# Optimization experiments

Measured on AMD Instinct MI355X. Metric: run time of the kernel, lower is better.

Reference implementation:

```python
import jax, jax.numpy as jnp
import numpy as np

N_NODES = 50000
N_EDGES = 600000
D = 128          # in_dim == hiddim
C = 40           # n_classes
L = 4            # n GCN layers
EPS = 1e-5       # BatchNorm1d default eps


def setup_inputs() -> dict:
    key = jax.random.key(0)
    ks = jax.random.split(key, 5)
    h = jax.random.normal(ks[0], (N_NODES, D), jnp.float32)
    src = jax.random.randint(ks[1], (N_EDGES,), 0, N_NODES, jnp.int32)
    dst = jax.random.randint(ks[2], (N_EDGES,), 0, N_NODES, jnp.int32)
    # learned parameters
    bn_gamma = jnp.ones((D,), jnp.float32)
    bn_beta = jnp.zeros((D,), jnp.float32)
    W1 = jax.random.normal(ks[3], (D, D), jnp.float32) * (1.0 / np.sqrt(D))
    b1 = jnp.zeros((D,), jnp.float32)
    bn2_gamma = jnp.ones((D,), jnp.float32)
    bn2_beta = jnp.zeros((D,), jnp.float32)
    W2 = jax.random.normal(ks[4], (D, C), jnp.float32) * (1.0 / np.sqrt(D))
    b2 = jnp.zeros((C,), jnp.float32)
    return {"h": h, "src": src, "dst": dst,
            "bn_gamma": bn_gamma, "bn_beta": bn_beta,
            "W1": W1, "b1": b1,
            "bn2_gamma": bn2_gamma, "bn2_beta": bn2_beta,
            "W2": W2, "b2": b2}


def _batchnorm(x, gamma, beta):
    # BatchNorm1d in training mode: biased batch variance over the node axis
    mu = x.mean(axis=0)
    var = x.var(axis=0)
    return (x - mu) * jax.lax.rsqrt(var + EPS) * gamma + beta


def reference(h, src, dst, bn_gamma, bn_beta, W1, b1, bn2_gamma, bn2_beta, W2, b2):
    n = h.shape[0]
    # in-degrees from dst indices, clamped to >= 1 (matches g.in_degrees().clamp(min=1))
    deg = jax.ops.segment_sum(jnp.ones(dst.shape[0], jnp.float32), dst, num_segments=n)
    norm = jax.lax.rsqrt(jnp.maximum(deg, 1.0))[:, None]  # deg^{-0.5}, [N,1]
    # in_feat_dropout = 0.0 -> identity
    for _ in range(L):
        h = h * norm
        # copy_u + sum reducer: scatter-add source features into destination nodes
        h = jax.ops.segment_sum(h[src], dst, num_segments=n)
        h = h * norm
        h = jax.nn.relu(_batchnorm(h, bn_gamma, bn_beta))  # shared BN across layers
    # MultiLinearLayer: Linear -> BN -> Linear (activation=None)
    x = h @ W1 + b1
    x = _batchnorm(x, bn2_gamma, bn2_beta)
    return x @ W2 + b2
```

## Files before the change

### kernel.cpp

```cpp
#include <hip/hip_runtime.h>

#define N_NODESC 50000
#define N_EDGESC 600000
#define DDIM 128
#define NCLASS 40
#define BN_EPS 1e-5f
#define STAT_BLOCKS 196
#define GATHER_BLOCKS 2048
#define SORT_ROWS 128
#define SORT_CAP 2560
#define SORT_BLOCKS 391

typedef short bhalf8 __attribute__((ext_vector_type(8)));
typedef float f32x4 __attribute__((ext_vector_type(4)));

union ABfrag { bhalf8 v; unsigned short u[8]; uint4 q; };

__device__ inline float bflo(unsigned d) { return __builtin_bit_cast(float, d << 16); }
__device__ inline float bfhi(unsigned d) { return __builtin_bit_cast(float, d & 0xffff0000u); }
__device__ inline unsigned short f2bf(float f) {
    unsigned u = __builtin_bit_cast(unsigned, f);
    u += 0x7fffu + ((u >> 16) & 1u);
    return (unsigned short)(u >> 16);
}

__global__ __launch_bounds__(256) void deg_kernel(const int* __restrict__ dst, int* __restrict__ deg) {
    int e = blockIdx.x * 256 + threadIdx.x;
    if (e < N_EDGESC) atomicAdd(&deg[dst[e]], 1);
}

__global__ __launch_bounds__(256) void scan1_kernel(const int* __restrict__ deg,
                                                    int* __restrict__ rowptr,
                                                    int* __restrict__ blocksums) {
    __shared__ int sh[256];
    int t = threadIdx.x;
    int i = blockIdx.x * 256 + t;
    int v = (i < N_NODESC) ? deg[i] : 0;
    sh[t] = v;
    __syncthreads();
    #pragma unroll
    for (int off = 1; off < 256; off <<= 1) {
        int tv = (t >= off) ? sh[t - off] : 0;
        __syncthreads();
        sh[t] += tv;
        __syncthreads();
    }
    if (i < N_NODESC) rowptr[i] = sh[t] - v;
    if (t == 255) blocksums[blockIdx.x] = sh[255];
}

__global__ void scan2_kernel(const int* __restrict__ blocksums, int* __restrict__ blockoff) {
    __shared__ int sh[256];
    int t = threadIdx.x;
    int v = (t < STAT_BLOCKS) ? blocksums[t] : 0;
    sh[t] = v;
    __syncthreads();
    #pragma unroll
    for (int off = 1; off < 256; off <<= 1) {
        int tv = (t >= off) ? sh[t - off] : 0;
        __syncthreads();
        sh[t] += tv;
        __syncthreads();
    }
    blockoff[t] = sh[t] - v;
}

__global__ __launch_bounds__(256) void scan3_kernel(int* __restrict__ rowptr,
                                                    const int* __restrict__ blockoff,
                                                    const int* __restrict__ deg,
                                                    int* __restrict__ cursor,
                                                    float* __restrict__ nrm) {
    int i = blockIdx.x * 256 + threadIdx.x;
    if (i < N_NODESC) {
        int r = rowptr[i] + blockoff[blockIdx.x];
        rowptr[i] = r;
        cursor[i] = r;
        nrm[i] = rsqrtf(fmaxf((float)deg[i], 1.0f));
    }
    if (blockIdx.x == 0 && threadIdx.x == 0) rowptr[N_NODESC] = N_EDGESC;
}

__global__ __launch_bounds__(256) void fill_kernel(const int* __restrict__ src,
                                                   const int* __restrict__ dst,
                                                   int* __restrict__ cursor,
                                                   int* __restrict__ csr) {
    int e = blockIdx.x * 256 + threadIdx.x;
    if (e < N_EDGESC) {
        int d = dst[e];
        int p = atomicAdd(&cursor[d], 1);
        csr[p] = src[e];
    }
}

__global__ __launch_bounds__(128) void sortrows_kernel(const int* __restrict__ rowptr,
                                                       int* __restrict__ csr) {
    __shared__ int buf[SORT_CAP];
    int r0 = blockIdx.x * SORT_ROWS;
    int r1 = r0 + SORT_ROWS; if (r1 > N_NODESC) r1 = N_NODESC;
    int base = rowptr[r0];
    int end  = rowptr[r1];
    int cnt  = end - base;
    if (cnt <= SORT_CAP) {
        for (int j = threadIdx.x; j < cnt; j += 128) buf[j] = csr[base + j];
        __syncthreads();
        int i = r0 + threadIdx.x;
        if (i < r1) {
            int b = rowptr[i] - base, e = rowptr[i + 1] - base;
            for (int j = b + 1; j < e; j++) {
                int v = buf[j];
                int k = j - 1;
                while (k >= b && buf[k] > v) { buf[k + 1] = buf[k]; k--; }
                buf[k + 1] = v;
            }
        }
        __syncthreads();
        for (int j = threadIdx.x; j < cnt; j += 128) csr[base + j] = buf[j];
    } else {
        int i = r0 + threadIdx.x;
        if (i < r1) {
            int b = rowptr[i], e = rowptr[i + 1];
            for (int j = b + 1; j < e; j++) {
                int v = csr[j];
                int k = j - 1;
                while (k >= b && csr[k] > v) { csr[k + 1] = csr[k]; k--; }
                csr[k + 1] = v;
            }
        }
    }
}

__global__ __launch_bounds__(256) void hconv_kernel(const float* __restrict__ h,
                                                    unsigned short* __restrict__ out) {
    int i = blockIdx.x * 256 + threadIdx.x;
    if (i < N_NODESC * DDIM / 8) {
        float4 v0 = reinterpret_cast<const float4*>(h)[i * 2];
        float4 v1 = reinterpret_cast<const float4*>(h)[i * 2 + 1];
        uint4 p;
        p.x = (unsigned)f2bf(v0.x) | ((unsigned)f2bf(v0.y) << 16);
        p.y = (unsigned)f2bf(v0.z) | ((unsigned)f2bf(v0.w) << 16);
        p.z = (unsigned)f2bf(v1.x) | ((unsigned)f2bf(v1.y) << 16);
        p.w = (unsigned)f2bf(v1.z) | ((unsigned)f2bf(v1.w) << 16);
        reinterpret_cast<uint4*>(out)[i] = p;
    }
}

__global__ __launch_bounds__(256) void w1prep_kernel(const float* __restrict__ W1,
                                                     unsigned short* __restrict__ W1T) {
    int idx = blockIdx.x * 256 + threadIdx.x;
    if (idx < DDIM * DDIM) {
        int k = idx >> 7, n = idx & 127;
        W1T[n * DDIM + k] = f2bf(W1[idx]);
    }
}

template <bool BN>
__global__ __launch_bounds__(256) void gather_kernel(const unsigned short* __restrict__ in,
                                                     const float* __restrict__ nrm,
                                                     const int* __restrict__ rowptr,
                                                     const int* __restrict__ csr,
                                                     const float* __restrict__ mu,
                                                     const float* __restrict__ rstd,
                                                     const float* __restrict__ gamma,
                                                     const float* __restrict__ beta,
                                                     unsigned short* __restrict__ out) {
    int lane = threadIdx.x & 63;
    int wave = threadIdx.x >> 6;
    int q    = lane >> 4;
    int c    = lane & 15;
    float sc[8], sh[8];
    if (BN) {
        float4 m0 = *reinterpret_cast<const float4*>(mu + c * 8);
        float4 m1 = *reinterpret_cast<const float4*>(mu + c * 8 + 4);
        float4 r0 = *reinterpret_cast<const float4*>(rstd + c * 8);
        float4 r1 = *reinterpret_cast<const float4*>(rstd + c * 8 + 4);
        float4 g0 = *reinterpret_cast<const float4*>(gamma + c * 8);
        float4 g1 = *reinterpret_cast<const float4*>(gamma + c * 8 + 4);
        float4 b0 = *reinterpret_cast<const float4*>(beta + c * 8);
        float4 b1 = *reinterpret_cast<const float4*>(beta + c * 8 + 4);
        sc[0] = r0.x * g0.x; sc[1] = r0.y * g0.y; sc[2] = r0.z * g0.z; sc[3] = r0.w * g0.w;
        sc[4] = r1.x * g1.x; sc[5] = r1.y * g1.y; sc[6] = r1.z * g1.z; sc[7] = r1.w * g1.w;
        sh[0] = b0.x - m0.x * sc[0]; sh[1] = b0.y - m0.y * sc[1];
        sh[2] = b0.z - m0.z * sc[2]; sh[3] = b0.w - m0.w * sc[3];
        sh[4] = b1.x - m1.x * sc[4]; sh[5] = b1.y - m1.y * sc[5];
        sh[6] = b1.z - m1.z * sc[6]; sh[7] = b1.w - m1.w * sc[7];
    }
    for (int i = blockIdx.x * 4 + wave; i < N_NODESC; i += GATHER_BLOCKS * 4) {
        int b = rowptr[i], e = rowptr[i + 1];
        float a[8] = {0.f, 0.f, 0.f, 0.f, 0.f, 0.f, 0.f, 0.f};
        int j = b + q;
        if (j < e) {
            int sidx = csr[j];
            float ns  = nrm[sidx];
            uint4 d   = reinterpret_cast<const uint4*>(in + (size_t)sidx * DDIM)[c];
            for (j += 4;; j += 4) {
                bool more = (j < e);
                int nsidx = 0; float nns = 0.f;
                uint4 nd = make_uint4(0u, 0u, 0u, 0u);
                if (more) {
                    nsidx = csr[j];
                    nns   = nrm[nsidx];
                    nd    = reinterpret_cast<const uint4*>(in + (size_t)nsidx * DDIM)[c];
                }
                float f[8];
                f[0] = bflo(d.x); f[1] = bfhi(d.x);
                f[2] = bflo(d.y); f[3] = bfhi(d.y);
                f[4] = bflo(d.z); f[5] = bfhi(d.z);
                f[6] = bflo(d.w); f[7] = bfhi(d.w);
                #pragma unroll
                for (int t = 0; t < 8; t++) {
                    float v = BN ? fmaxf(f[t] * sc[t] + sh[t], 0.f) : f[t];
                    a[t] += v * ns;
                }
                if (!more) break;
                d = nd; ns = nns;
            }
        }
        #pragma unroll
        for (int t = 0; t < 8; t++) a[t] += __shfl_xor(a[t], 16);
        #pragma unroll
        for (int t = 0; t < 8; t++) a[t] += __shfl_xor(a[t], 32);
        if (q == 0) {
            float ni = nrm[i];
            uint4 p;
            p.x = (unsigned)f2bf(a[0] * ni) | ((unsigned)f2bf(a[1] * ni) << 16);
            p.y = (unsigned)f2bf(a[2] * ni) | ((unsigned)f2bf(a[3] * ni) << 16);
            p.z = (unsigned)f2bf(a[4] * ni) | ((unsigned)f2bf(a[5] * ni) << 16);
            p.w = (unsigned)f2bf(a[6] * ni) | ((unsigned)f2bf(a[7] * ni) << 16);
            reinterpret_cast<uint4*>(out + (size_t)i * DDIM)[c] = p;
        }
    }
}

__global__ __launch_bounds__(256) void stats_bf16_kernel(const unsigned short* __restrict__ x,
                                                         float* __restrict__ partials) {
    __shared__ float sh[256];
    int c2 = threadIdx.x & 63;
    int rg = threadIdx.x >> 6;
    int row0 = blockIdx.x * 256;
    int rowEnd = row0 + 256; if (rowEnd > N_NODESC) rowEnd = N_NODESC;
    float s0 = 0.f, s1 = 0.f, q0 = 0.f, q1 = 0.f;
    for (int r = row0 + rg; r < rowEnd; r += 4) {
        unsigned d = reinterpret_cast<const unsigned*>(x + (size_t)r * DDIM)[c2];
        float f0 = bflo(d), f1 = bfhi(d);
        s0 += f0; q0 += f0 * f0;
        s1 += f1; q1 += f1 * f1;
    }
    sh[threadIdx.x] = s0; __syncthreads();
    if (rg == 0) s0 += sh[64 + c2] + sh[128 + c2] + sh[192 + c2];
    __syncthreads();
    sh[threadIdx.x] = s1; __syncthreads();
    if (rg == 0) s1 += sh[64 + c2] + sh[128 + c2] + sh[192 + c2];
    __syncthreads();
    sh[threadIdx.x] = q0; __syncthreads();
    if (rg == 0) q0 += sh[64 + c2] + sh[128 + c2] + sh[192 + c2];
    __syncthreads();
    sh[threadIdx.x] = q1; __syncthreads();
    if (rg == 0) {
        q1 += sh[64 + c2] + sh[128 + c2] + sh[192 + c2];
        partials[blockIdx.x * 256 + 2 * c2]           = s0;
        partials[blockIdx.x * 256 + 2 * c2 + 1]       = s1;
        partials[blockIdx.x * 256 + 128 + 2 * c2]     = q0;
        partials[blockIdx.x * 256 + 128 + 2 * c2 + 1] = q1;
    }
}

__global__ __launch_bounds__(256) void stats_f32_kernel(const float* __restrict__ x,
                                                        float* __restrict__ partials) {
    __shared__ float sh[256];
    int col = threadIdx.x & 127;
    int grp = threadIdx.x >> 7;
    int rowEnd = (blockIdx.x + 1) * 256;
    if (rowEnd > N_NODESC) rowEnd = N_NODESC;
    float s = 0.f, q = 0.f;
    for (int r = blockIdx.x * 256 + grp; r < rowEnd; r += 2) {
        float v = x[(size_t)r * DDIM + col];
        s += v;
        q += v * v;
    }
    sh[threadIdx.x] = s;
    __syncthreads();
    float s2 = (grp == 0) ? (s + sh[128 + col]) : 0.f;
    __syncthreads();
    sh[threadIdx.x] = q;
    __syncthreads();
    if (grp == 0) {
        float q2 = q + sh[128 + col];
        partials[blockIdx.x * 256 + col]       = s2;
        partials[blockIdx.x * 256 + 128 + col] = q2;
    }
}

__global__ __launch_bounds__(1024) void finalize_kernel(const float* __restrict__ partials,
                                                        float* __restrict__ mu, float* __restrict__ rstd) {
    __shared__ double shd[2048];
    int col = threadIdx.x & 127;
    int sl  = threadIdx.x >> 7;
    double s = 0.0, q = 0.0;
    for (int b = sl; b < STAT_BLOCKS; b += 8) {
        s += (double)partials[b * 256 + col];
        q += (double)partials[b * 256 + 128 + col];
    }
    shd[threadIdx.x] = s;
    shd[1024 + threadIdx.x] = q;
    __syncthreads();
    if (sl == 0) {
        #pragma unroll
        for (int k = 1; k < 8; k++) {
            s += shd[k * 128 + col];
            q += shd[1024 + k * 128 + col];
        }
        double m = s / (double)N_NODESC;
        double v = q / (double)N_NODESC - m * m;
        if (v < 0.0) v = 0.0;
        mu[col]   = (float)m;
        rstd[col] = rsqrtf((float)v + BN_EPS);
    }
}

__global__ __launch_bounds__(256) void linear1_mfma(const unsigned short* __restrict__ Qb,
                                                    const unsigned short* __restrict__ W1T,
                                                    const float* __restrict__ b1,
                                                    const float* __restrict__ mu,
                                                    const float* __restrict__ rstd,
                                                    const float* __restrict__ gamma,
                                                    const float* __restrict__ beta,
                                                    float* __restrict__ X) {
    __shared__ uint4 wlds[2048];
    __shared__ float scs[DDIM], shs[DDIM], bias[DDIM];
    int tid = threadIdx.x;
    for (int i = tid; i < 2048; i += 256) {
        uint4 v = reinterpret_cast<const uint4*>(W1T)[i];
        int o = i << 4;
        int n = o >> 8;
        int sw = (o & 255) ^ ((n & 7) << 4);
        wlds[(n << 4) | (sw >> 4)] = v;
    }
    if (tid < DDIM) {
        float a = rstd[tid] * gamma[tid];
        scs[tid] = a;
        shs[tid] = beta[tid] - mu[tid] * a;
        bias[tid] = b1[tid];
    }
    __syncthreads();
    int wave = tid >> 6, lane = tid & 63;
    int l15 = lane & 15, l4 = lane >> 4;
    int tile = blockIdx.x * 4 + wave;
    if (tile >= 3128) return;
    int row0 = tile * 16;
    int arow = row0 + l15; if (arow >= N_NODESC) arow = N_NODESC - 1;
    const uint4* aptr = reinterpret_cast<const uint4*>(Qb + (size_t)arow * DDIM);
    f32x4 acc[8];
    #pragma unroll
    for (int cf = 0; cf < 8; cf++) acc[cf] = (f32x4){0.f, 0.f, 0.f, 0.f};
    #pragma unroll
    for (int ks = 0; ks < 4; ks++) {
        uint4 ad = aptr[ks * 4 + l4];
        int kb = ks * 32 + l4 * 8;
        ABfrag a;
        float f;
        f = bflo(ad.x); a.u[0] = f2bf(fmaxf(f * scs[kb + 0] + shs[kb + 0], 0.f));
        f = bfhi(ad.x); a.u[1] = f2bf(fmaxf(f * scs[kb + 1] + shs[kb + 1], 0.f));
        f = bflo(ad.y); a.u[2] = f2bf(fmaxf(f * scs[kb + 2] + shs[kb + 2], 0.f));
        f = bfhi(ad.y); a.u[3] = f2bf(fmaxf(f * scs[kb + 3] + shs[kb + 3], 0.f));
        f = bflo(ad.z); a.u[4] = f2bf(fmaxf(f * scs[kb + 4] + shs[kb + 4], 0.f));
        f = bfhi(ad.z); a.u[5] = f2bf(fmaxf(f * scs[kb + 5] + shs[kb + 5], 0.f));
        f = bflo(ad.w); a.u[6] = f2bf(fmaxf(f * scs[kb + 6] + shs[kb + 6], 0.f));
        f = bfhi(ad.w); a.u[7] = f2bf(fmaxf(f * scs[kb + 7] + shs[kb + 7], 0.f));
        int koff = ks * 64 + l4 * 16;
        #pragma unroll
        for (int cf = 0; cf < 8; cf++) {
            int n = cf * 16 + l15;
            ABfrag b;
            b.q = wlds[(n << 4) | ((koff ^ ((n & 7) << 4)) >> 4)];
            acc[cf] = __builtin_amdgcn_mfma_f32_16x16x32_bf16(a.v, b.v, acc[cf], 0, 0, 0);
        }
    }
    #pragma unroll
    for (int cf = 0; cf < 8; cf++) {
        int col = cf * 16 + l15;
        float bb = bias[col];
        #pragma unroll
        for (int r = 0; r < 4; r++) {
            int row = row0 + l4 * 4 + r;
            if (row < N_NODESC) X[(size_t)row * DDIM + col] = acc[cf][r] + bb;
        }
    }
}

__global__ void fold_kernel(const float* __restrict__ W2, const float* __restrict__ b2,
                            const float* __restrict__ g2, const float* __restrict__ be2,
                            const float* __restrict__ mu2, const float* __restrict__ rstd2,
                            float* __restrict__ W2f, float* __restrict__ b2f) {
    __shared__ float s[DDIM], t[DDIM];
    int tid = threadIdx.x;
    if (tid < DDIM) {
        float sc = rstd2[tid] * g2[tid];
        s[tid] = sc;
        t[tid] = be2[tid] - mu2[tid] * sc;
    }
    __syncthreads();
    for (int idx = tid; idx < DDIM * NCLASS; idx += 256) {
        int k = idx / NCLASS;
        W2f[idx] = W2[idx] * s[k];
    }
    if (tid < NCLASS) {
        float acc = b2[tid];
        for (int k = 0; k < DDIM; k++) acc += t[k] * W2[k * NCLASS + tid];
        b2f[tid] = acc;
    }
}

#define L2_TILE 64
__global__ __launch_bounds__(256) void linear2_kernel(const float* __restrict__ X,
                                                      const float* __restrict__ W2f,
                                                      const float* __restrict__ b2f,
                                                      float* __restrict__ out) {
    __shared__ float Ws[DDIM][NCLASS];
    for (int idx = threadIdx.x; idx < DDIM * NCLASS; idx += 256) {
        (&Ws[0][0])[idx] = W2f[idx];
    }
    __syncthreads();
    int cg = threadIdx.x & 7;
    int rp = threadIdx.x >> 3;
    int c0 = cg * 5;
    for (int base = blockIdx.x * L2_TILE; base < N_NODESC; base += gridDim.x * L2_TILE) {
        int row0 = base + rp * 2;
        int row1 = row0 + 1;
        int r0c = row0 < N_NODESC ? row0 : (N_NODESC - 1);
        int r1c = row1 < N_NODESC ? row1 : (N_NODESC - 1);
        const float* r0p = X + (size_t)r0c * DDIM;
        const float* r1p = X + (size_t)r1c * DDIM;
        float a0[5] = {0.f, 0.f, 0.f, 0.f, 0.f};
        float a1[5] = {0.f, 0.f, 0.f, 0.f, 0.f};
        #pragma unroll 4
        for (int k4 = 0; k4 < DDIM; k4 += 4) {
            float4 x0 = *reinterpret_cast<const float4*>(r0p + k4);
            float4 x1 = *reinterpret_cast<const float4*>(r1p + k4);
            #pragma unroll
            for (int j = 0; j < 5; j++) {
                float w0 = Ws[k4 + 0][c0 + j];
                float w1 = Ws[k4 + 1][c0 + j];
                float w2 = Ws[k4 + 2][c0 + j];
                float w3 = Ws[k4 + 3][c0 + j];
                a0[j] += w0 * x0.x + w1 * x0.y + w2 * x0.z + w3 * x0.w;
                a1[j] += w0 * x1.x + w1 * x1.y + w2 * x1.z + w3 * x1.w;
            }
        }
        if (row0 < N_NODESC) {
            #pragma unroll
            for (int j = 0; j < 5; j++) out[(size_t)row0 * NCLASS + c0 + j] = a0[j] + b2f[c0 + j];
        }
        if (row1 < N_NODESC) {
            #pragma unroll
            for (int j = 0; j < 5; j++) out[(size_t)row1 * NCLASS + c0 + j] = a1[j] + b2f[c0 + j];
        }
    }
}

extern "C" void kernel_launch(void* const* d_in, const int* in_sizes, int n_in,
                              void* d_out, int out_size, void* d_ws, size_t ws_size,
                              hipStream_t stream) {
    const float* h    = (const float*)d_in[0];
    const int*   src  = (const int*)d_in[1];
    const int*   dst  = (const int*)d_in[2];
    const float* bn_g = (const float*)d_in[3];
    const float* bn_b = (const float*)d_in[4];
    const float* W1   = (const float*)d_in[5];
    const float* b1   = (const float*)d_in[6];
    const float* g2   = (const float*)d_in[7];
    const float* be2  = (const float*)d_in[8];
    const float* W2   = (const float*)d_in[9];
    const float* b2   = (const float*)d_in[10];
    float* out = (float*)d_out;

    float* ws      = (float*)d_ws;
    float* nrm     = ws;
    int*   deg     = (int*)(ws + N_NODESC);
    int*   cursor  = deg + N_NODESC;
    int*   rowptr  = cursor + N_NODESC;
    int*   bsums   = rowptr + 50016;
    int*   boff    = bsums + 256;
    int*   csr     = boff + 256;
    float* partials = (float*)(csr + N_EDGESC);
    float* mu      = partials + STAT_BLOCKS * 256;
    float* rstd    = mu + DDIM;
    float* W2f     = rstd + DDIM;
    float* b2f     = W2f + DDIM * NCLASS;
    unsigned short* W1T = (unsigned short*)(b2f + 64);
    unsigned short* Hb  = (unsigned short*)((float*)W1T + 8192);
    unsigned short* Pb  = (unsigned short*)((float*)Hb + 3200000);
    float* X       = (float*)((float*)Pb + 3200000);

    (void)in_sizes; (void)n_in; (void)out_size; (void)ws_size;

    hipMemsetAsync(deg, 0, N_NODESC * sizeof(int), stream);
    deg_kernel<<<(N_EDGESC + 255) / 256, 256, 0, stream>>>(dst, deg);
    scan1_kernel<<<STAT_BLOCKS, 256, 0, stream>>>(deg, rowptr, bsums);
    scan2_kernel<<<1, 256, 0, stream>>>(bsums, boff);
    scan3_kernel<<<STAT_BLOCKS, 256, 0, stream>>>(rowptr, boff, deg, cursor, nrm);
    fill_kernel<<<(N_EDGESC + 255) / 256, 256, 0, stream>>>(src, dst, cursor, csr);
    sortrows_kernel<<<SORT_BLOCKS, 128, 0, stream>>>(rowptr, csr);
    hconv_kernel<<<(N_NODESC * DDIM / 8 + 255) / 256, 256, 0, stream>>>(h, Hb);
    w1prep_kernel<<<(DDIM * DDIM + 255) / 256, 256, 0, stream>>>(W1, W1T);

    gather_kernel<false><<<GATHER_BLOCKS, 256, 0, stream>>>(Hb, nrm, rowptr, csr,
                                                            nullptr, nullptr, nullptr, nullptr, Pb);
    stats_bf16_kernel<<<STAT_BLOCKS, 256, 0, stream>>>(Pb, partials);
    finalize_kernel<<<1, 1024, 0, stream>>>(partials, mu, rstd);
    gather_kernel<true><<<GATHER_BLOCKS, 256, 0, stream>>>(Pb, nrm, rowptr, csr,
                                                           mu, rstd, bn_g, bn_b, Hb);
    stats_bf16_kernel<<<STAT_BLOCKS, 256, 0, stream>>>(Hb, partials);
    finalize_kernel<<<1, 1024, 0, stream>>>(partials, mu, rstd);
    gather_kernel<true><<<GATHER_BLOCKS, 256, 0, stream>>>(Hb, nrm, rowptr, csr,
                                                           mu, rstd, bn_g, bn_b, Pb);
    stats_bf16_kernel<<<STAT_BLOCKS, 256, 0, stream>>>(Pb, partials);
    finalize_kernel<<<1, 1024, 0, stream>>>(partials, mu, rstd);
    gather_kernel<true><<<GATHER_BLOCKS, 256, 0, stream>>>(Pb, nrm, rowptr, csr,
                                                           mu, rstd, bn_g, bn_b, Hb);
    stats_bf16_kernel<<<STAT_BLOCKS, 256, 0, stream>>>(Hb, partials);
    finalize_kernel<<<1, 1024, 0, stream>>>(partials, mu, rstd);

    linear1_mfma<<<782, 256, 0, stream>>>(Hb, W1T, b1, mu, rstd, bn_g, bn_b, X);
    stats_f32_kernel<<<STAT_BLOCKS, 256, 0, stream>>>(X, partials);
    finalize_kernel<<<1, 1024, 0, stream>>>(partials, mu, rstd);
    fold_kernel<<<1, 256, 0, stream>>>(W2, b2, g2, be2, mu, rstd, W2f, b2f);
    linear2_kernel<<<512, 256, 0, stream>>>(X, W2f, b2f, out);
}
```

Baseline: 429.4 us.

## Fuse BatchNorm statistics into gather and linear1 kernels, column-chunk the gather

The separate stats passes over each layer output are removed. BatchNorm sum and sum-of-squares are now accumulated inside the gather kernel and the linear1 MFMA kernel, which write per-block partials for new finalize kernels. The gather is also restructured so each block handles one 32-column chunk of the feature dimension, with 16 edge slots per wave, which changes how memory is accessed. This saves a full re-read of the activations per layer but adds shuffles and LDS reductions, and statistics are now computed from fp32 values rather than the stored bf16.

After: 626.6 us. 1.46x slower.

```diff
diff --git a/kernel.cpp b/kernel.cpp
--- a/kernel.cpp
+++ b/kernel.cpp
@@ -6,7 +6,9 @@
 #define NCLASS 40
 #define BN_EPS 1e-5f
 #define STAT_BLOCKS 196
+#define CHUNK_BLOCKS 512
 #define GATHER_BLOCKS 2048
+#define L1_BLOCKS 782
 #define SORT_ROWS 128
 #define SORT_CAP 2560
 #define SORT_BLOCKS 391
@@ -162,21 +164,27 @@
                                                      const float* __restrict__ rstd,
                                                      const float* __restrict__ gamma,
                                                      const float* __restrict__ beta,
-                                                     unsigned short* __restrict__ out) {
-    int lane = threadIdx.x & 63;
-    int wave = threadIdx.x >> 6;
-    int q    = lane >> 4;
-    int c    = lane & 15;
+                                                     unsigned short* __restrict__ out,
+                                                     float* __restrict__ partials) {
+    __shared__ float red[4][64];
+    int bx    = blockIdx.x;
+    int chunk = bx >> 9;
+    int blk   = bx & (CHUNK_BLOCKS - 1);
+    int lane  = threadIdx.x & 63;
+    int wave  = threadIdx.x >> 6;
+    int slot  = lane >> 2;
+    int cl    = lane & 3;
+    int colbase = chunk * 32 + cl * 8;
     float sc[8], sh[8];
     if (BN) {
-        float4 m0 = *reinterpret_cast<const float4*>(mu + c * 8);
-        float4 m1 = *reinterpret_cast<const float4*>(mu + c * 8 + 4);
-        float4 r0 = *reinterpret_cast<const float4*>(rstd + c * 8);
-        float4 r1 = *reinterpret_cast<const float4*>(rstd + c * 8 + 4);
-        float4 g0 = *reinterpret_cast<const float4*>(gamma + c * 8);
-        float4 g1 = *reinterpret_cast<const float4*>(gamma + c * 8 + 4);
-        float4 b0 = *reinterpret_cast<const float4*>(beta + c * 8);
-        float4 b1 = *reinterpret_cast<const float4*>(beta + c * 8 + 4);
+        float4 m0 = *reinterpret_cast<const float4*>(mu + colbase);
+        float4 m1 = *reinterpret_cast<const float4*>(mu + colbase + 4);
+        float4 r0 = *reinterpret_cast<const float4*>(rstd + colbase);
+        float4 r1 = *reinterpret_cast<const float4*>(rstd + colbase + 4);
+        float4 g0 = *reinterpret_cast<const float4*>(gamma + colbase);
+        float4 g1 = *reinterpret_cast<const float4*>(gamma + colbase + 4);
+        float4 b0 = *reinterpret_cast<const float4*>(beta + colbase);
+        float4 b1 = *reinterpret_cast<const float4*>(beta + colbase + 4);
         sc[0] = r0.x * g0.x; sc[1] = r0.y * g0.y; sc[2] = r0.z * g0.z; sc[3] = r0.w * g0.w;
         sc[4] = r1.x * g1.x; sc[5] = r1.y * g1.y; sc[6] = r1.z * g1.z; sc[7] = r1.w * g1.w;
         sh[0] = b0.x - m0.x * sc[0]; sh[1] = b0.y - m0.y * sc[1];
@@ -184,121 +192,101 @@
         sh[4] = b1.x - m1.x * sc[4]; sh[5] = b1.y - m1.y * sc[5];
         sh[6] = b1.z - m1.z * sc[6]; sh[7] = b1.w - m1.w * sc[7];
     }
-    for (int i = blockIdx.x * 4 + wave; i < N_NODESC; i += GATHER_BLOCKS * 4) {
+    float ssum[8] = {0.f,0.f,0.f,0.f,0.f,0.f,0.f,0.f};
+    float sqr[8]  = {0.f,0.f,0.f,0.f,0.f,0.f,0.f,0.f};
+    for (int i = blk * 4 + wave; i < N_NODESC; i += GATHER_BLOCKS / 4 * 4) {
         int b = rowptr[i], e = rowptr[i + 1];
-        float a[8] = {0.f, 0.f, 0.f, 0.f, 0.f, 0.f, 0.f, 0.f};
-        int j = b + q;
-        if (j < e) {
+        float a[8] = {0.f,0.f,0.f,0.f,0.f,0.f,0.f,0.f};
+        for (int j = b + slot; j < e; j += 16) {
             int sidx = csr[j];
-            float ns  = nrm[sidx];
-            uint4 d   = reinterpret_cast<const uint4*>(in + (size_t)sidx * DDIM)[c];
-            for (j += 4;; j += 4) {
-                bool more = (j < e);
-                int nsidx = 0; float nns = 0.f;
-                uint4 nd = make_uint4(0u, 0u, 0u, 0u);
-                if (more) {
-                    nsidx = csr[j];
-                    nns   = nrm[nsidx];
-                    nd    = reinterpret_cast<const uint4*>(in + (size_t)nsidx * DDIM)[c];
-                }
-                float f[8];
-                f[0] = bflo(d.x); f[1] = bfhi(d.x);
-                f[2] = bflo(d.y); f[3] = bfhi(d.y);
-                f[4] = bflo(d.z); f[5] = bfhi(d.z);
-                f[6] = bflo(d.w); f[7] = bfhi(d.w);
-                #pragma unroll
-                for (int t = 0; t < 8; t++) {
-                    float v = BN ? fmaxf(f[t] * sc[t] + sh[t], 0.f) : f[t];
-                    a[t] += v * ns;
-                }
-                if (!more) break;
-                d = nd; ns = nns;
+            float ns = nrm[sidx];
+            uint4 d = *reinterpret_cast<const uint4*>(in + (size_t)sidx * DDIM + colbase);
+            float f[8];
+            f[0] = bflo(d.x); f[1] = bfhi(d.x);
+            f[2] = bflo(d.y); f[3] = bfhi(d.y);
+            f[4] = bflo(d.z); f[5] = bfhi(d.z);
+            f[6] = bflo(d.w); f[7] = bfhi(d.w);
+            #pragma unroll
+            for (int t = 0; t < 8; t++) {
+                float v = BN ? fmaxf(f[t] * sc[t] + sh[t], 0.f) : f[t];
+                a[t] += v * ns;
             }
         }
         #pragma unroll
-        for (int t = 0; t < 8; t++) a[t] += __shfl_xor(a[t], 16);
-        #pragma unroll
-        for (int t = 0; t < 8; t++) a[t] += __shfl_xor(a[t], 32);
-        if (q == 0) {
+        for (int t = 0; t < 8; t++) {
+            a[t] += __shfl_xor(a[t], 4);
+            a[t] += __shfl_xor(a[t], 8);
+            a[t] += __shfl_xor(a[t], 16);
+            a[t] += __shfl_xor(a[t], 32);
+        }
+        if (slot == 0) {
             float ni = nrm[i];
+            #pragma unroll
+            for (int t = 0; t < 8; t++) {
+                a[t] *= ni;
+                ssum[t] += a[t];
+                sqr[t]  += a[t] * a[t];
+            }
             uint4 p;
-            p.x = (unsigned)f2bf(a[0] * ni) | ((unsigned)f2bf(a[1] * ni) << 16);
-            p.y = (unsigned)f2bf(a[2] * ni) | ((unsigned)f2bf(a[3] * ni) << 16);
-            p.z = (unsigned)f2bf(a[4] * ni) | ((unsigned)f2bf(a[5] * ni) << 16);
-            p.w = (unsigned)f2bf(a[6] * ni) | ((unsigned)f2bf(a[7] * ni) << 16);
-            reinterpret_cast<uint4*>(out + (size_t)i * DDIM)[c] = p;
-        }
-    }
-}
-
-__global__ __launch_bounds__(256) void stats_bf16_kernel(const unsigned short* __restrict__ x,
-                                                         float* __restrict__ partials) {
-    __shared__ float sh[256];
-    int c2 = threadIdx.x & 63;
-    int rg = threadIdx.x >> 6;
-    int row0 = blockIdx.x * 256;
-    int rowEnd = row0 + 256; if (rowEnd > N_NODESC) rowEnd = N_NODESC;
-    float s0 = 0.f, s1 = 0.f, q0 = 0.f, q1 = 0.f;
-    for (int r = row0 + rg; r < rowEnd; r += 4) {
-        unsigned d = reinterpret_cast<const unsigned*>(x + (size_t)r * DDIM)[c2];
-        float f0 = bflo(d), f1 = bfhi(d);
-        s0 += f0; q0 += f0 * f0;
-        s1 += f1; q1 += f1 * f1;
-    }
-    sh[threadIdx.x] = s0; __syncthreads();
-    if (rg == 0) s0 += sh[64 + c2] + sh[128 + c2] + sh[192 + c2];
-    __syncthreads();
-    sh[threadIdx.x] = s1; __syncthreads();
-    if (rg == 0) s1 += sh[64 + c2] + sh[128 + c2] + sh[192 + c2];
-    __syncthreads();
-    sh[threadIdx.x] = q0; __syncthreads();
-    if (rg == 0) q0 += sh[64 + c2] + sh[128 + c2] + sh[192 + c2];
-    __syncthreads();
-    sh[threadIdx.x] = q1; __syncthreads();
-    if (rg == 0) {
-        q1 += sh[64 + c2] + sh[128 + c2] + sh[192 + c2];
-        partials[blockIdx.x * 256 + 2 * c2]           = s0;
-        partials[blockIdx.x * 256 + 2 * c2 + 1]       = s1;
-        partials[blockIdx.x * 256 + 128 + 2 * c2]     = q0;
-        partials[blockIdx.x * 256 + 128 + 2 * c2 + 1] = q1;
-    }
-}
-
-__global__ __launch_bounds__(256) void stats_f32_kernel(const float* __restrict__ x,
-                                                        float* __restrict__ partials) {
-    __shared__ float sh[256];
+            p.x = (unsigned)f2bf(a[0]) | ((unsigned)f2bf(a[1]) << 16);
+            p.y = (unsigned)f2bf(a[2]) | ((unsigned)f2bf(a[3]) << 16);
+            p.z = (unsigned)f2bf(a[4]) | ((unsigned)f2bf(a[5]) << 16);
+            p.w = (unsigned)f2bf(a[6]) | ((unsigned)f2bf(a[7]) << 16);
+            *reinterpret_cast<uint4*>(out + (size_t)i * DDIM + colbase) = p;
+        }
+    }
+    if (slot == 0) {
+        #pragma unroll
+        for (int t = 0; t < 8; t++) {
+            red[wave][cl * 8 + t]      = ssum[t];
+            red[wave][32 + cl * 8 + t] = sqr[t];
+        }
+    }
+    __syncthreads();
+    int tid = threadIdx.x;
+    if (tid < 64) {
+        partials[(size_t)bx * 64 + tid] = red[0][tid] + red[1][tid] + red[2][tid] + red[3][tid];
+    }
+}
+
+__global__ __launch_bounds__(1024) void finalize_g_kernel(const float* __restrict__ partials,
+                                                          float* __restrict__ mu, float* __restrict__ rstd) {
+    __shared__ double shd[2048];
     int col = threadIdx.x & 127;
-    int grp = threadIdx.x >> 7;
-    int rowEnd = (blockIdx.x + 1) * 256;
-    if (rowEnd > N_NODESC) rowEnd = N_NODESC;
-    float s = 0.f, q = 0.f;
-    for (int r = blockIdx.x * 256 + grp; r < rowEnd; r += 2) {
-        float v = x[(size_t)r * DDIM + col];
-        s += v;
-        q += v * v;
-    }
-    sh[threadIdx.x] = s;
-    __syncthreads();
-    float s2 = (grp == 0) ? (s + sh[128 + col]) : 0.f;
-    __syncthreads();
-    sh[threadIdx.x] = q;
-    __syncthreads();
-    if (grp == 0) {
-        float q2 = q + sh[128 + col];
-        partials[blockIdx.x * 256 + col]       = s2;
-        partials[blockIdx.x * 256 + 128 + col] = q2;
-    }
-}
-
-__global__ __launch_bounds__(1024) void finalize_kernel(const float* __restrict__ partials,
-                                                        float* __restrict__ mu, float* __restrict__ rstd) {
+    int sl  = threadIdx.x >> 7;
+    int ch  = col >> 5, c32 = col & 31;
+    double s = 0.0, q = 0.0;
+    for (int b = sl; b < CHUNK_BLOCKS; b += 8) {
+        const float* p = partials + (size_t)(ch * CHUNK_BLOCKS + b) * 64;
+        s += (double)p[c32];
+        q += (double)p[32 + c32];
+    }
+    shd[threadIdx.x] = s;
+    shd[1024 + threadIdx.x] = q;
+    __syncthreads();
+    if (sl == 0) {
+        #pragma unroll
+        for (int k = 1; k < 8; k++) {
+            s += shd[k * 128 + col];
+            q += shd[1024 + k * 128 + col];
+        }
+        double m = s / (double)N_NODESC;
+        double v = q / (double)N_NODESC - m * m;
+        if (v < 0.0) v = 0.0;
+        mu[col]   = (float)m;
+        rstd[col] = rsqrtf((float)v + BN_EPS);
+    }
+}
+
+__global__ __launch_bounds__(1024) void finalize_l1_kernel(const float* __restrict__ partials,
+                                                           float* __restrict__ mu, float* __restrict__ rstd) {
     __shared__ double shd[2048];
     int col = threadIdx.x & 127;
     int sl  = threadIdx.x >> 7;
     double s = 0.0, q = 0.0;
-    for (int b = sl; b < STAT_BLOCKS; b += 8) {
-        s += (double)partials[b * 256 + col];
-        q += (double)partials[b * 256 + 128 + col];
+    for (int b = sl; b < L1_BLOCKS; b += 8) {
+        s += (double)partials[(size_t)b * 256 + col];
+        q += (double)partials[(size_t)b * 256 + 128 + col];
     }
     shd[threadIdx.x] = s;
     shd[1024 + threadIdx.x] = q;
@@ -324,9 +312,11 @@
                                                     const float* __restrict__ rstd,
                                                     const float* __restrict__ gamma,
                                                     const float* __restrict__ beta,
-                                                    float* __restrict__ X) {
+                                                    float* __restrict__ X,
+                                                    float* __restrict__ partials) {
     __shared__ uint4 wlds[2048];
     __shared__ float scs[DDIM], shs[DDIM], bias[DDIM];
+    __shared__ float red[4][256];
     int tid = threadIdx.x;
     for (int i = tid; i < 2048; i += 256) {
         uint4 v = reinterpret_cast<const uint4*>(W1T)[i];
@@ -345,7 +335,6 @@
     int wave = tid >> 6, lane = tid & 63;
     int l15 = lane & 15, l4 = lane >> 4;
     int tile = blockIdx.x * 4 + wave;
-    if (tile >= 3128) return;
     int row0 = tile * 16;
     int arow = row0 + l15; if (arow >= N_NODESC) arow = N_NODESC - 1;
     const uint4* aptr = reinterpret_cast<const uint4*>(Qb + (size_t)arow * DDIM);
@@ -375,15 +364,36 @@
             acc[cf] = __builtin_amdgcn_mfma_f32_16x16x32_bf16(a.v, b.v, acc[cf], 0, 0, 0);
         }
     }
+    float cs[8], cq[8];
     #pragma unroll
     for (int cf = 0; cf < 8; cf++) {
         int col = cf * 16 + l15;
         float bb = bias[col];
+        float sl_ = 0.f, ql_ = 0.f;
         #pragma unroll
         for (int r = 0; r < 4; r++) {
             int row = row0 + l4 * 4 + r;
-            if (row < N_NODESC) X[(size_t)row * DDIM + col] = acc[cf][r] + bb;
-        }
+            float x = acc[cf][r] + bb;
+            if (row < N_NODESC) {
+                X[(size_t)row * DDIM + col] = x;
+                sl_ += x;
+                ql_ += x * x;
+            }
+        }
+        sl_ += __shfl_xor(sl_, 16); sl_ += __shfl_xor(sl_, 32);
+        ql_ += __shfl_xor(ql_, 16); ql_ += __shfl_xor(ql_, 32);
+        cs[cf] = sl_; cq[cf] = ql_;
+    }
+    if (l4 == 0) {
+        #pragma unroll
+        for (int cf = 0; cf < 8; cf++) {
+            red[wave][cf * 16 + l15]       = cs[cf];
+            red[wave][128 + cf * 16 + l15] = cq[cf];
+        }
+    }
+    __syncthreads();
+    if (tid < 256) {
+        partials[(size_t)blockIdx.x * 256 + tid] = red[0][tid] + red[1][tid] + red[2][tid] + red[3][tid];
     }
 }
 
@@ -482,7 +492,7 @@
     int*   boff    = bsums + 256;
     int*   csr     = boff + 256;
     float* partials = (float*)(csr + N_EDGESC);
-    float* mu      = partials + STAT_BLOCKS * 256;
+    float* mu      = partials + 200192;
     float* rstd    = mu + DDIM;
     float* W2f     = rstd + DDIM;
     float* b2f     = W2f + DDIM * NCLASS;
@@ -504,25 +514,20 @@
     w1prep_kernel<<<(DDIM * DDIM + 255) / 256, 256, 0, stream>>>(W1, W1T);
 
     gather_kernel<false><<<GATHER_BLOCKS, 256, 0, stream>>>(Hb, nrm, rowptr, csr,
-                                                            nullptr, nullptr, nullptr, nullptr, Pb);
-    stats_bf16_kernel<<<STAT_BLOCKS, 256, 0, stream>>>(Pb, partials);
-    finalize_kernel<<<1, 1024, 0, stream>>>(partials, mu, rstd);
+                                                            nullptr, nullptr, nullptr, nullptr, Pb, partials);
+    finalize_g_kernel<<<1, 1024, 0, stream>>>(partials, mu, rstd);
     gather_kernel<true><<<GATHER_BLOCKS, 256, 0, stream>>>(Pb, nrm, rowptr, csr,
-                                                           mu, rstd, bn_g, bn_b, Hb);
-    stats_bf16_kernel<<<STAT_BLOCKS, 256, 0, stream>>>(Hb, partials);
-    finalize_kernel<<<1, 1024, 0, stream>>>(partials, mu, rstd);
+                                                           mu, rstd, bn_g, bn_b, Hb, partials);
+    finalize_g_kernel<<<1, 1024, 0, stream>>>(partials, mu, rstd);
     gather_kernel<true><<<GATHER_BLOCKS, 256, 0, stream>>>(Hb, nrm, rowptr, csr,
-                                                           mu, rstd, bn_g, bn_b, Pb);
-    stats_bf16_kernel<<<STAT_BLOCKS, 256, 0, stream>>>(Pb, partials);
-    finalize_kernel<<<1, 1024, 0, stream>>>(partials, mu, rstd);
+                                                           mu, rstd, bn_g, bn_b, Pb, partials);
+    finalize_g_kernel<<<1, 1024, 0, stream>>>(partials, mu, rstd);
     gather_kernel<true><<<GATHER_BLOCKS, 256, 0, stream>>>(Pb, nrm, rowptr, csr,
-                                                           mu, rstd, bn_g, bn_b, Hb);
-    stats_bf16_kernel<<<STAT_BLOCKS, 256, 0, stream>>>(Hb, partials);
-    finalize_kernel<<<1, 1024, 0, stream>>>(partials, mu, rstd);
-
-    linear1_mfma<<<782, 256, 0, stream>>>(Hb, W1T, b1, mu, rstd, bn_g, bn_b, X);
-    stats_f32_kernel<<<STAT_BLOCKS, 256, 0, stream>>>(X, partials);
-    finalize_kernel<<<1, 1024, 0, stream>>>(partials, mu, rstd);
+                                                           mu, rstd, bn_g, bn_b, Hb, partials);
+    finalize_g_kernel<<<1, 1024, 0, stream>>>(partials, mu, rstd);
+
+    linear1_mfma<<<L1_BLOCKS, 256, 0, stream>>>(Hb, W1T, b1, mu, rstd, bn_g, bn_b, X, partials);
+    finalize_l1_kernel<<<1, 1024, 0, stream>>>(partials, mu, rstd);
     fold_kernel<<<1, 256, 0, stream>>>(W2, b2, g2, be2, mu, rstd, W2f, b2f);
     linear2_kernel<<<512, 256, 0, stream>>>(X, W2f, b2f, out);
 }
```
